# Optimization experiments

Measured on AMD Instinct MI355X. Metric: run time of the kernel, lower is better.

## Reference

```python
import jax, jax.numpy as jnp
import numpy as np

N = 50000
E = 800000
IN = 128
H = 128
OUT = 64
L = 2
THETA = 1.0
SCALE = 2.0


def setup_inputs() -> dict:
    key = jax.random.key(0)
    ks = jax.random.split(key, 12)
    g = lambda k, s: (jax.random.normal(k, s, jnp.float32) * 0.05)
    return {
        "x": jax.random.normal(ks[0], (N, IN), jnp.float32),
        "edge_index": jax.random.randint(ks[1], (2, E), 0, N),
        "mlp_w1": g(ks[2], (IN, 512)), "mlp_b1": jnp.zeros((512,), jnp.float32),
        "mlp_w2": g(ks[3], (512, 64)), "mlp_b2": jnp.zeros((64,), jnp.float32),
        "mlp_w3": g(ks[4], (64, OUT)), "mlp_b3": jnp.zeros((OUT,), jnp.float32),
        "parsing": jnp.ones((L, OUT, OUT), jnp.float32) / SCALE,
        "lin0_w": g(ks[5], (IN, H)), "lin0_b": jnp.zeros((H,), jnp.float32),
        "lin1_w": g(ks[6], (H, OUT)), "lin1_b": jnp.zeros((OUT,), jnp.float32),
        "conv_w1": g(ks[7], (L, H, H)),
        "conv_w2": g(ks[8], (L, H, H)),
    }


def reference(x, edge_index, mlp_w1, mlp_b1, mlp_w2, mlp_b2, mlp_w3, mlp_b3,
              parsing, lin0_w, lin0_b, lin1_w, lin1_b, conv_w1, conv_w2):
    row, col = edge_index[0], edge_index[1]  # start, end

    # --- learn_soft_edge3 (algebraically exact reduction of outer-product + bmm + diag) ---
    h = jax.nn.relu(x @ mlp_w1 + mlp_b1)
    h = jax.nn.relu(h @ mlp_w2 + mlp_b2)
    logits = h @ mlp_w3 + mlp_b3                      # [N, OUT]
    P = jax.nn.relu(SCALE * parsing[0])               # [OUT, OUT]
    # diag(outer(start,end) @ P)[e,c] = start[e,c] * (end @ P)[e,c]
    ew = jnp.sum(logits[row] * (logits @ P)[col], axis=1)  # [E]
    mean = ew.mean()
    var = jnp.var(ew, ddof=1)                          # torch.var is unbiased
    ew = (ew - mean) * jnp.sqrt(jnp.float32(1e-4) / var) + 1.0

    # --- GCN2 stack ---
    x0 = jax.nn.relu(x @ lin0_w + lin0_b)              # [N, H]
    # gcn_norm with self loops (weight 1)
    loop = jnp.arange(N)
    r = jnp.concatenate([row, loop])
    c = jnp.concatenate([col, loop])
    w = jnp.concatenate([ew, jnp.ones((N,), ew.dtype)])
    deg = jax.ops.segment_sum(w, c, num_segments=N)
    dinv = jnp.where(deg > 0, jax.lax.rsqrt(jnp.where(deg > 0, deg, 1.0)), 0.0)
    norm = dinv[r] * w * dinv[c]                       # [E+N]

    hcur = x0
    alpha = 0.0
    for ln in range(L):
        agg = jax.ops.segment_sum(norm[:, None] * hcur[r], c, num_segments=N)  # [N, H]
        agg = agg * (1.0 - alpha)
        x0a = alpha * x0
        beta = float(np.log(THETA / (ln + 1) + 1.0))
        out = (1.0 - beta) * agg + beta * (agg @ conv_w1[ln]) \
            + (1.0 - beta) * x0a + beta * (x0a @ conv_w2[ln])
        hcur = jax.nn.relu(out)
    return hcur @ lin1_w + lin1_b                      # [N, OUT]
```

## Files before the change

### kernel.cpp

```cpp
#include <hip/hip_runtime.h>
#include <hip/hip_bf16.h>
#include <hip/hip_fp16.h>
#include <math.h>

#define NN 50000
#define NE 800000

typedef __attribute__((ext_vector_type(8))) short bf16x8;
typedef __attribute__((ext_vector_type(4))) float f32x4;

__device__ __forceinline__ short f2bf(float f){
  unsigned u = __float_as_uint(f);
  unsigned r = (u + 0x7fffu + ((u >> 16) & 1u)) >> 16;
  return (short)r;
}
__device__ __forceinline__ float bf2f(short s){
  return __uint_as_float(((unsigned)(unsigned short)s) << 16);
}

__device__ __forceinline__ unsigned f2fp8(float f){
  __half h = __float2half(f * 0.00390625f);
  unsigned hb = (unsigned)__half_as_ushort(h);
  unsigned s = hb >> 15;
  unsigned mag = hb & 0x7fffu;
  mag = mag + 0x3fu + ((mag >> 7) & 1u);
  unsigned m8 = mag >> 7;
  if (m8 > 0x7eu) m8 = 0x7eu;
  return (s << 7) | m8;
}
__device__ __forceinline__ void fp8x4_dec(unsigned u, float2& lo, float2& hi){
  unsigned l = ((u & 0x80u) << 8) | ((u & 0x7fu) << 7)
             | ((u & 0x8000u) << 16) | ((u & 0x7f00u) << 15);
  unsigned h = ((u & 0x800000u) >> 8) | ((u & 0x7f0000u) >> 9)
             | (u & 0x80000000u) | ((u & 0x7f000000u) >> 1);
  __half2 hl = *(__half2*)&l;
  __half2 hh = *(__half2*)&h;
  lo = __half22float2(hl);
  hi = __half22float2(hh);
}
__device__ __forceinline__ float fp8_dot4(unsigned a, unsigned b){
  float2 al, ah, bl, bh;
  fp8x4_dec(a, al, ah); fp8x4_dec(b, bl, bh);
  return al.x*bl.x + al.y*bl.y + ah.x*bh.x + ah.y*bh.y;
}

__global__ __launch_bounds__(256) void zero_cnt_k(int* __restrict__ cnt, float* __restrict__ scal, int n){
  int i = blockIdx.x*256 + threadIdx.x;
  if (i < n) cnt[i] = 0;
  if (blockIdx.x == 0 && threadIdx.x < 16) scal[threadIdx.x] = 0.0f;
}

__global__ __launch_bounds__(256) void prep_k(const float* __restrict__ w1,
    const float* __restrict__ w2, const float* __restrict__ w3, const float* __restrict__ pars,
    const float* __restrict__ lin0w, const float* __restrict__ cw1, const float* __restrict__ lin1w,
    short* __restrict__ w1t, short* __restrict__ w2t, short* __restrict__ w3t, short* __restrict__ Pt,
    short* __restrict__ lin0wt, short* __restrict__ cw1t0, short* __restrict__ cw1t1,
    short* __restrict__ lin1wt){
  int idx = blockIdx.x*256 + threadIdx.x;
  if (idx < 65536){
    int n = idx >> 7, k = idx & 127;
    w1t[idx] = f2bf(w1[k*512 + n]);
  } else if (idx < 98304){
    int i = idx - 65536; int n = i >> 9, k = i & 511;
    w2t[i] = f2bf(w2[k*64 + n]);
  } else if (idx < 102400){
    int i = idx - 98304; int n = i >> 6, k = i & 63;
    w3t[i] = f2bf(w3[k*64 + n]);
  } else if (idx < 106496){
    int i = idx - 102400; int n = i >> 6, k = i & 63;
    Pt[i] = f2bf(fmaxf(2.f*pars[k*64 + n], 0.f));
  } else if (idx < 122880){
    int i = idx - 106496; int n = i >> 7, k = i & 127;
    lin0wt[i] = f2bf(lin0w[k*128 + n]);
  } else if (idx < 139264){
    int i = idx - 122880; int n = i >> 7, k = i & 127;
    cw1t0[i] = f2bf(cw1[k*128 + n]);
  } else if (idx < 155648){
    int i = idx - 139264; int n = i >> 7, k = i & 127;
    cw1t1[i] = f2bf(cw1[16384 + k*128 + n]);
  } else if (idx < 163840){
    int i = idx - 155648; int n = i >> 7, k = i & 127;
    lin1wt[i] = f2bf(lin1w[k*64 + n]);
  }
}

__global__ __launch_bounds__(256) void mlp_mfma_k(
    const float* __restrict__ x,
    const short* __restrict__ w1t, const float* __restrict__ b1,
    const short* __restrict__ w2t, const float* __restrict__ b2,
    const short* __restrict__ w3t, const float* __restrict__ b3,
    const short* __restrict__ Pt,
    unsigned char* __restrict__ lg8, unsigned char* __restrict__ lgp8,
    short* __restrict__ xb, int M)
{
  __shared__ short xs [32][136];
  __shared__ short h1s[32][520];
  __shared__ short h2s[32][72];
  __shared__ short lgs[32][72];
  const int t = threadIdx.x;
  const int wave = t >> 6, lane = t & 63;
  const int quad = lane >> 4, l16 = lane & 15;
  const int m0 = blockIdx.x * 32;

  for (int task = t; task < 512; task += 256){
    int row = task >> 4, c0 = (task & 15) * 8;
    float4 v0 = make_float4(0,0,0,0), v1 = v0;
    if (m0 + row < M){
      v0 = *(const float4*)(x + (size_t)(m0+row)*128 + c0);
      v1 = *(const float4*)(x + (size_t)(m0+row)*128 + c0 + 4);
    }
    bf16x8 s;
    s[0]=f2bf(v0.x); s[1]=f2bf(v0.y); s[2]=f2bf(v0.z); s[3]=f2bf(v0.w);
    s[4]=f2bf(v1.x); s[5]=f2bf(v1.y); s[6]=f2bf(v1.z); s[7]=f2bf(v1.w);
    *(bf16x8*)&xs[row][c0] = s;
  }
  __syncthreads();

  {
    f32x4 acc[2][8];
    #pragma unroll
    for (int mt=0;mt<2;mt++)
      #pragma unroll
      for (int nt=0;nt<8;nt++) acc[mt][nt] = (f32x4){0.f,0.f,0.f,0.f};
    for (int k0 = 0; k0 < 128; k0 += 32){
      bf16x8 a0 = *(const bf16x8*)&xs[l16     ][k0 + quad*8];
      bf16x8 a1 = *(const bf16x8*)&xs[16 + l16][k0 + quad*8];
      #pragma unroll
      for (int nt = 0; nt < 8; nt++){
        int n = wave*128 + nt*16 + l16;
        bf16x8 b = *(const bf16x8*)(w1t + (size_t)n*128 + k0 + quad*8);
        acc[0][nt] = __builtin_amdgcn_mfma_f32_16x16x32_bf16(a0, b, acc[0][nt], 0,0,0);
        acc[1][nt] = __builtin_amdgcn_mfma_f32_16x16x32_bf16(a1, b, acc[1][nt], 0,0,0);
      }
    }
    #pragma unroll
    for (int nt = 0; nt < 8; nt++){
      int n = wave*128 + nt*16 + l16;
      float bb = b1[n];
      #pragma unroll
      for (int mt = 0; mt < 2; mt++){
        #pragma unroll
        for (int r = 0; r < 4; r++){
          int row = mt*16 + quad*4 + r;
          h1s[row][n] = f2bf(fmaxf(acc[mt][nt][r] + bb, 0.f));
        }
      }
    }
  }
  __syncthreads();

  {
    f32x4 acc[2];
    acc[0] = (f32x4){0.f,0.f,0.f,0.f}; acc[1] = acc[0];
    const int n = wave*16 + l16;
    for (int k0 = 0; k0 < 512; k0 += 32){
      bf16x8 b  = *(const bf16x8*)(w2t + (size_t)n*512 + k0 + quad*8);
      bf16x8 a0 = *(const bf16x8*)&h1s[l16     ][k0 + quad*8];
      bf16x8 a1 = *(const bf16x8*)&h1s[16 + l16][k0 + quad*8];
      acc[0] = __builtin_amdgcn_mfma_f32_16x16x32_bf16(a0, b, acc[0], 0,0,0);
      acc[1] = __builtin_amdgcn_mfma_f32_16x16x32_bf16(a1, b, acc[1], 0,0,0);
    }
    float bb = b2[n];
    #pragma unroll
    for (int mt = 0; mt < 2; mt++)
      #pragma unroll
      for (int r = 0; r < 4; r++)
        h2s[mt*16 + quad*4 + r][n] = f2bf(fmaxf(acc[mt][r] + bb, 0.f));
  }
  __syncthreads();

  {
    f32x4 acc[2];
    acc[0] = (f32x4){0.f,0.f,0.f,0.f}; acc[1] = acc[0];
    const int n = wave*16 + l16;
    for (int k0 = 0; k0 < 64; k0 += 32){
      bf16x8 b  = *(const bf16x8*)(w3t + (size_t)n*64 + k0 + quad*8);
      bf16x8 a0 = *(const bf16x8*)&h2s[l16     ][k0 + quad*8];
      bf16x8 a1 = *(const bf16x8*)&h2s[16 + l16][k0 + quad*8];
      acc[0] = __builtin_amdgcn_mfma_f32_16x16x32_bf16(a0, b, acc[0], 0,0,0);
      acc[1] = __builtin_amdgcn_mfma_f32_16x16x32_bf16(a1, b, acc[1], 0,0,0);
    }
    float bb = b3[n];
    #pragma unroll
    for (int mt = 0; mt < 2; mt++)
      #pragma unroll
      for (int r = 0; r < 4; r++)
        lgs[mt*16 + quad*4 + r][n] = f2bf(acc[mt][r] + bb);
  }
  __syncthreads();

  {
    f32x4 acc[2];
    acc[0] = (f32x4){0.f,0.f,0.f,0.f}; acc[1] = acc[0];
    const int n = wave*16 + l16;
    for (int k0 = 0; k0 < 64; k0 += 32){
      bf16x8 b  = *(const bf16x8*)(Pt + (size_t)n*64 + k0 + quad*8);
      bf16x8 a0 = *(const bf16x8*)&lgs[l16     ][k0 + quad*8];
      bf16x8 a1 = *(const bf16x8*)&lgs[16 + l16][k0 + quad*8];
      acc[0] = __builtin_amdgcn_mfma_f32_16x16x32_bf16(a0, b, acc[0], 0,0,0);
      acc[1] = __builtin_amdgcn_mfma_f32_16x16x32_bf16(a1, b, acc[1], 0,0,0);
    }
    #pragma unroll
    for (int mt = 0; mt < 2; mt++)
      #pragma unroll
      for (int r = 0; r < 4; r++)
        h2s[mt*16 + quad*4 + r][n] = f2bf(acc[mt][r]);
  }
  __syncthreads();

  {
    int row = t >> 3, c0 = (t & 7) * 8;
    int gm = m0 + row;
    if (gm < M){
      const short* pl = &lgs[row][c0];
      const short* pp = &h2s[row][c0];
      unsigned a0 = 0, a1 = 0, b0 = 0, b1 = 0;
      #pragma unroll
      for (int j = 0; j < 4; j++){
        a0 |= f2fp8(bf2f(pl[j]))     << (8*j);
        a1 |= f2fp8(bf2f(pl[4+j]))   << (8*j);
        b0 |= f2fp8(bf2f(pp[j]))     << (8*j);
        b1 |= f2fp8(bf2f(pp[4+j]))   << (8*j);
      }
      uint2 av; av.x = a0; av.y = a1;
      uint2 bv; bv.x = b0; bv.y = b1;
      *(uint2*)(lg8  + (size_t)gm*64 + c0) = av;
      *(uint2*)(lgp8 + (size_t)gm*64 + c0) = bv;
    }
  }
  for (int task = t; task < 512; task += 256){
    int row = task >> 4, c0 = (task & 15) * 8;
    int gm = m0 + row;
    if (gm < M)
      *(bf16x8*)(xb + (size_t)gm*128 + c0) = *(const bf16x8*)&xs[row][c0];
  }
}

template<int NT, bool RELU, bool RESID, bool BF16OUT>
__global__ __launch_bounds__(256) void bgemm_k(
    const short* __restrict__ A, const short* __restrict__ Bt,
    const float* __restrict__ bias, const short* __restrict__ extra,
    float* __restrict__ C, short* __restrict__ Cb, int M, float beta)
{
  const int N = NT*64;
  __shared__ short As[32][136];
  const int t = threadIdx.x;
  const int wave = t >> 6, lane = t & 63;
  const int quad = lane >> 4, l16 = lane & 15;
  const int m0 = blockIdx.x * 32;

  for (int task = t; task < 512; task += 256){
    int row = task >> 4, c0 = (task & 15) * 8;
    bf16x8 v = {0,0,0,0,0,0,0,0};
    if (m0 + row < M) v = *(const bf16x8*)(A + (size_t)(m0+row)*128 + c0);
    *(bf16x8*)&As[row][c0] = v;
  }
  __syncthreads();

  f32x4 acc[2][NT];
  #pragma unroll
  for (int mt=0;mt<2;mt++)
    #pragma unroll
    for (int nt=0;nt<NT;nt++) acc[mt][nt] = (f32x4){0.f,0.f,0.f,0.f};

  #pragma unroll
  for (int k0 = 0; k0 < 128; k0 += 32){
    bf16x8 a0 = *(const bf16x8*)&As[l16     ][k0 + quad*8];
    bf16x8 a1 = *(const bf16x8*)&As[16 + l16][k0 + quad*8];
    #pragma unroll
    for (int nt = 0; nt < NT; nt++){
      int n = (wave*NT + nt)*16 + l16;
      bf16x8 b = *(const bf16x8*)(Bt + (size_t)n*128 + k0 + quad*8);
      acc[0][nt] = __builtin_amdgcn_mfma_f32_16x16x32_bf16(a0, b, acc[0][nt], 0,0,0);
      acc[1][nt] = __builtin_amdgcn_mfma_f32_16x16x32_bf16(a1, b, acc[1][nt], 0,0,0);
    }
  }

  #pragma unroll
  for (int nt = 0; nt < NT; nt++){
    int n = (wave*NT + nt)*16 + l16;
    float bb = (bias != nullptr) ? bias[n] : 0.f;
    #pragma unroll
    for (int mt = 0; mt < 2; mt++){
      #pragma unroll
      for (int r = 0; r < 4; r++){
        int gm = m0 + mt*16 + quad*4 + r;
        if (gm >= M) continue;
        float v = acc[mt][nt][r];
        if (RESID){
          float ex = bf2f(extra[(size_t)gm*N + n]);
          v = beta*v + (1.f - beta)*ex;
        }
        v += bb;
        if (RELU) v = fmaxf(v, 0.f);
        if (BF16OUT) Cb[(size_t)gm*N + n] = f2bf(v);
        else         C [(size_t)gm*N + n] = v;
      }
    }
  }
}

__global__ __launch_bounds__(256) void count_k(const int* __restrict__ col, int* __restrict__ cnt,
    int* __restrict__ rank, int E){
  int i = (blockIdx.x*256 + threadIdx.x)*4;
  if (i + 3 < E){
    int4 c = *(const int4*)(col + i);
    int r0 = atomicAdd(&cnt[c.x], 1);
    int r1 = atomicAdd(&cnt[c.y], 1);
    int r2 = atomicAdd(&cnt[c.z], 1);
    int r3 = atomicAdd(&cnt[c.w], 1);
    *(int4*)(rank + i) = make_int4(r0, r1, r2, r3);
  } else {
    for (; i < E; i++) rank[i] = atomicAdd(&cnt[col[i]], 1);
  }
}

__global__ __launch_bounds__(256) void scan_sums_k(const int* __restrict__ cnt, int* __restrict__ bsum, int n){
  __shared__ int s[256];
  const int t = threadIdx.x;
  int i = blockIdx.x*1024 + t*4;
  int4 v = make_int4(0,0,0,0);
  if (i + 3 < n) v = *(const int4*)(cnt + i);
  else {
    if (i   < n) v.x = cnt[i];
    if (i+1 < n) v.y = cnt[i+1];
    if (i+2 < n) v.z = cnt[i+2];
    if (i+3 < n) v.w = cnt[i+3];
  }
  s[t] = v.x + v.y + v.z + v.w;
  __syncthreads();
  for (int st = 128; st; st >>= 1){
    if (t < st) s[t] += s[t + st];
    __syncthreads();
  }
  if (t == 0) bsum[blockIdx.x] = s[0];
}

__global__ __launch_bounds__(64) void scan_bsum_k(int* __restrict__ bsum, int nb){
  int t = threadIdx.x;
  int own = (t < nb) ? bsum[t] : 0;
  int v = own;
  #pragma unroll
  for (int off = 1; off < 64; off <<= 1){
    int o = __shfl_up(v, off, 64);
    if (t >= off) v += o;
  }
  if (t < nb) bsum[t] = v - own;
}

__global__ __launch_bounds__(256) void scan_final_k(const int* __restrict__ cnt, const int* __restrict__ bsum,
    int* __restrict__ off, int n, int total){
  __shared__ int s[256];
  const int t = threadIdx.x;
  int i = blockIdx.x*1024 + t*4;
  int4 v = make_int4(0,0,0,0);
  if (i + 3 < n) v = *(const int4*)(cnt + i);
  else {
    if (i   < n) v.x = cnt[i];
    if (i+1 < n) v.y = cnt[i+1];
    if (i+2 < n) v.z = cnt[i+2];
    if (i+3 < n) v.w = cnt[i+3];
  }
  int tsum = v.x + v.y + v.z + v.w;
  s[t] = tsum;
  __syncthreads();
  #pragma unroll
  for (int st = 1; st < 256; st <<= 1){
    int a = (t >= st) ? s[t - st] : 0;
    __syncthreads();
    s[t] += a;
    __syncthreads();
  }
  int base = s[t] - tsum + bsum[blockIdx.x];
  int o0 = base, o1 = o0 + v.x, o2 = o1 + v.y, o3 = o2 + v.z;
  if (i   < n) off[i]   = o0;
  if (i+1 < n) off[i+1] = o1;
  if (i+2 < n) off[i+2] = o2;
  if (i+3 < n) off[i+3] = o3;
  if (blockIdx.x == 0 && t == 0) off[n] = total;
}

__global__ __launch_bounds__(256) void scatter_k(const int* __restrict__ row, const int* __restrict__ col,
    const int* __restrict__ off, const int* __restrict__ rank,
    int2* __restrict__ csr_sd, int E){
  int i = (blockIdx.x*256 + threadIdx.x)*4;
  if (i + 3 < E){
    int4 r = *(const int4*)(row + i);
    int4 c = *(const int4*)(col + i);
    int4 k = *(const int4*)(rank + i);
    int o0 = off[c.x], o1 = off[c.y], o2 = off[c.z], o3 = off[c.w];
    int2 p0; p0.x = r.x; p0.y = c.x;
    int2 p1; p1.x = r.y; p1.y = c.y;
    int2 p2; p2.x = r.z; p2.y = c.z;
    int2 p3; p3.x = r.w; p3.y = c.w;
    csr_sd[o0 + k.x] = p0;
    csr_sd[o1 + k.y] = p1;
    csr_sd[o2 + k.z] = p2;
    csr_sd[o3 + k.w] = p3;
  } else {
    for (; i < E; i++){
      int2 p; p.x = row[i]; p.y = col[i];
      csr_sd[off[col[i]] + rank[i]] = p;
    }
  }
}

__global__ __launch_bounds__(256) void ew2_k(const unsigned char* __restrict__ lg8,
    const unsigned char* __restrict__ lgp8,
    const int2* __restrict__ sd,
    float* __restrict__ w, float* __restrict__ scal, int E){
  const int t = threadIdx.x;
  const int lane = t & 63, wid = t >> 6;
  const int g = lane >> 4, q = lane & 15;
  const int gid = (blockIdx.x*4 + wid)*4 + g;
  const int ngroups = gridDim.x*16;
  float s = 0.f, ss = 0.f;
  for (int base = gid*4; base < E; base += ngroups*4){
    int4 p01 = *(const int4*)(sd + base);
    int4 p23 = *(const int4*)(sd + base + 2);
    unsigned a0 = *(const unsigned*)(lg8  + (size_t)p01.x*64 + q*4);
    unsigned a1 = *(const unsigned*)(lg8  + (size_t)p01.z*64 + q*4);
    unsigned a2 = *(const unsigned*)(lg8  + (size_t)p23.x*64 + q*4);
    unsigned a3 = *(const unsigned*)(lg8  + (size_t)p23.z*64 + q*4);
    unsigned b0 = *(const unsigned*)(lgp8 + (size_t)p01.y*64 + q*4);
    unsigned b1 = *(const unsigned*)(lgp8 + (size_t)p01.w*64 + q*4);
    unsigned b2 = *(const unsigned*)(lgp8 + (size_t)p23.y*64 + q*4);
    unsigned b3 = *(const unsigned*)(lgp8 + (size_t)p23.w*64 + q*4);
    float v0 = fp8_dot4(a0, b0);
    float v1 = fp8_dot4(a1, b1);
    float v2 = fp8_dot4(a2, b2);
    float v3 = fp8_dot4(a3, b3);
    #pragma unroll
    for (int o = 1; o < 16; o <<= 1){
      v0 += __shfl_xor(v0, o); v1 += __shfl_xor(v1, o);
      v2 += __shfl_xor(v2, o); v3 += __shfl_xor(v3, o);
    }
    if (q == 0){
      float4 vv = make_float4(v0*65536.f, v1*65536.f, v2*65536.f, v3*65536.f);
      *(float4*)(w + base) = vv;
      s  += vv.x + vv.y + vv.z + vv.w;
      ss += vv.x*vv.x + vv.y*vv.y + vv.z*vv.z + vv.w*vv.w;
    }
  }
  #pragma unroll
  for (int o = 1; o < 64; o <<= 1){ s += __shfl_xor(s, o); ss += __shfl_xor(ss, o); }
  __shared__ float ls[4], lss[4];
  if (lane == 0){ ls[wid] = s; lss[wid] = ss; }
  __syncthreads();
  if (t == 0){
    atomicAdd(&scal[0], ls[0]+ls[1]+ls[2]+ls[3]);
    atomicAdd(&scal[1], lss[0]+lss[1]+lss[2]+lss[3]);
  }
}

__global__ void finalize_k(float* scal, int E){
  double sum = (double)scal[0], sumsq = (double)scal[1];
  double mean = sum / (double)E;
  double var  = (sumsq - sum*sum/(double)E) / (double)(E-1);
  scal[2] = (float)mean;
  scal[3] = (float)sqrt(1e-4 / var);
}

__global__ __launch_bounds__(256) void degnorm_k(float* __restrict__ w, const int* __restrict__ off,
    const float* __restrict__ scal, float* __restrict__ dinv, int Nn){
  int n = blockIdx.x*256 + threadIdx.x;
  if (n < Nn){
    float mean = scal[2], k = scal[3];
    int s = off[n], e = off[n+1];
    float d = 1.0f;
    for (int j = s; j < e; j++){
      float v = (w[j] - mean) * k + 1.0f;
      w[j] = v;
      d += v;
    }
    dinv[n] = (d > 0.f) ? rsqrtf(d) : 0.f;
  }
}

__global__ __launch_bounds__(256) void wfin_k(float* __restrict__ w, const int2* __restrict__ sd,
    const float* __restrict__ dinv, int E){
  int i = (blockIdx.x*256 + threadIdx.x)*4;
  if (i + 3 < E){
    int4 p01 = *(const int4*)(sd + i);
    int4 p23 = *(const int4*)(sd + i + 2);
    float4 wv = *(const float4*)(w + i);
    float d0 = dinv[p01.x]*dinv[p01.y];
    float d1 = dinv[p01.z]*dinv[p01.w];
    float d2 = dinv[p23.x]*dinv[p23.y];
    float d3 = dinv[p23.z]*dinv[p23.w];
    wv.x *= d0; wv.y *= d1; wv.z *= d2; wv.w *= d3;
    *(float4*)(w + i) = wv;
  } else {
    for (; i < E; i++){
      int2 p = sd[i];
      w[i] = w[i] * dinv[p.y] * dinv[p.x];
    }
  }
}

__global__ __launch_bounds__(256) void agg_gather_k(const short* __restrict__ hb,
    const int* __restrict__ off, const int2* __restrict__ sd, const float* __restrict__ w,
    const float* __restrict__ dinv, short* __restrict__ aggb, int Nn){
  int n = blockIdx.x*4 + (threadIdx.x >> 6);
  int lane = threadIdx.x & 63;
  if (n >= Nn) return;
  float d = dinv[n];
  short2 hv = *(const short2*)(hb + (size_t)n*128 + lane*2);
  float acc0 = d*d*bf2f(hv.x), acc1 = d*d*bf2f(hv.y);
  int s = off[n], e = off[n+1];
  int j = s;
  for (; j + 7 < e; j += 8){
    int4 p0 = *(const int4*)(sd + j);
    int4 p1 = *(const int4*)(sd + j + 2);
    int4 p2 = *(const int4*)(sd + j + 4);
    int4 p3 = *(const int4*)(sd + j + 6);
    float4 w0 = *(const float4*)(w + j);
    float4 w1 = *(const float4*)(w + j + 4);
    short2 h0 = *(const short2*)(hb + (size_t)p0.x*128 + lane*2);
    short2 h1 = *(const short2*)(hb + (size_t)p0.z*128 + lane*2);
    short2 h2 = *(const short2*)(hb + (size_t)p1.x*128 + lane*2);
    short2 h3 = *(const short2*)(hb + (size_t)p1.z*128 + lane*2);
    short2 h4 = *(const short2*)(hb + (size_t)p2.x*128 + lane*2);
    short2 h5 = *(const short2*)(hb + (size_t)p2.z*128 + lane*2);
    short2 h6 = *(const short2*)(hb + (size_t)p3.x*128 + lane*2);
    short2 h7 = *(const short2*)(hb + (size_t)p3.z*128 + lane*2);
    acc0 += w0.x*bf2f(h0.x) + w0.y*bf2f(h1.x) + w0.z*bf2f(h2.x) + w0.w*bf2f(h3.x)
          + w1.x*bf2f(h4.x) + w1.y*bf2f(h5.x) + w1.z*bf2f(h6.x) + w1.w*bf2f(h7.x);
    acc1 += w0.x*bf2f(h0.y) + w0.y*bf2f(h1.y) + w0.z*bf2f(h2.y) + w0.w*bf2f(h3.y)
          + w1.x*bf2f(h4.y) + w1.y*bf2f(h5.y) + w1.z*bf2f(h6.y) + w1.w*bf2f(h7.y);
  }
  for (; j < e; j++){
    int2 p = sd[j];
    short2 h0 = *(const short2*)(hb + (size_t)p.x*128 + lane*2);
    float w0 = w[j];
    acc0 += w0*bf2f(h0.x); acc1 += w0*bf2f(h0.y);
  }
  short2 o; o.x = f2bf(acc0); o.y = f2bf(acc1);
  *(short2*)(aggb + (size_t)n*128 + lane*2) = o;
}

extern "C" void kernel_launch(void* const* d_in, const int* in_sizes, int n_in,
                              void* d_out, int out_size, void* d_ws, size_t ws_size,
                              hipStream_t stream){
  const float* x      = (const float*)d_in[0];
  const int*   ei     = (const int*)  d_in[1];
  const float* w1     = (const float*)d_in[2];
  const float* b1     = (const float*)d_in[3];
  const float* w2     = (const float*)d_in[4];
  const float* b2     = (const float*)d_in[5];
  const float* w3     = (const float*)d_in[6];
  const float* b3     = (const float*)d_in[7];
  const float* pars   = (const float*)d_in[8];
  const float* lin0w  = (const float*)d_in[9];
  const float* lin0b  = (const float*)d_in[10];
  const float* lin1w  = (const float*)d_in[11];
  const float* lin1b  = (const float*)d_in[12];
  const float* cw1    = (const float*)d_in[13];
  float* out          = (float*)d_out;

  float* ws = (float*)d_ws;
  int*   cnt     = (int*)(ws + 0);
  int*   off     = (int*)(ws + 50048);
  int2*  csr_sd  = (int2*)(ws + 150144);
  int*   bsum    = (int*)(ws + 1750400);
  short* lin0wt  = (short*)(ws + 1751000);
  short* cw1t0   = lin0wt + 16384;
  short* cw1t1   = cw1t0 + 16384;
  short* lin1wt  = cw1t1 + 16384;
  unsigned char* lg8  = (unsigned char*)(ws + 1800000);
  unsigned char* lgp8 = (unsigned char*)(ws + 2600000);
  float* csr_w2  = ws + 3400000;
  float* dinv    = ws + 5800000;
  float* scal    = ws + 5850048;
  short* bufAb   = (short*)(ws + 5900000);
  short* bufCb   = (short*)(ws + 9100000);
  short* aggb    = (short*)(ws + 12300000);
  short* bufBb   = (short*)(ws + 15500000);
  short* w1t     = (short*)(ws + 18700000);
  short* w2t     = w1t + 65536;
  short* w3t     = w2t + 32768;
  short* Pt      = w3t + 4096;
  short* xb      = (short*)(ws + 18800000);
  int*   rank    = (int*)(ws + 22000000);

  const int Mn = NN, E = NE;
  const int* erow = ei;
  const int* ecol = ei + E;
  const float beta0 = 0.69314718055994530942f;
  const float beta1 = 0.40546510810816438198f;
  const int nScanB = (Mn + 1023) / 1024;
  const int nGB = (Mn + 31) / 32;
  const int nE4 = (E/4 + 255) / 256;

  zero_cnt_k<<<(Mn+255)/256, 256, 0, stream>>>(cnt, scal, Mn);
  prep_k<<<(163840+255)/256, 256, 0, stream>>>(w1, w2, w3, pars, lin0w, cw1, lin1w,
                                               w1t, w2t, w3t, Pt, lin0wt, cw1t0, cw1t1, lin1wt);
  count_k<<<nE4, 256, 0, stream>>>(ecol, cnt, rank, E);
  scan_sums_k<<<nScanB, 256, 0, stream>>>(cnt, bsum, Mn);
  scan_bsum_k<<<1, 64, 0, stream>>>(bsum, nScanB);
  scan_final_k<<<nScanB, 256, 0, stream>>>(cnt, bsum, off, Mn, E);
  scatter_k<<<nE4, 256, 0, stream>>>(erow, ecol, off, rank, csr_sd, E);
  mlp_mfma_k<<<(Mn+31)/32, 256, 0, stream>>>(x, w1t, b1, w2t, b2, w3t, b3, Pt,
                                             lg8, lgp8, xb, Mn);
  ew2_k<<<1024, 256, 0, stream>>>(lg8, lgp8, csr_sd, csr_w2, scal, E);
  finalize_k<<<1, 1, 0, stream>>>(scal, E);
  degnorm_k<<<(Mn+255)/256, 256, 0, stream>>>(csr_w2, off, scal, dinv, Mn);
  wfin_k<<<nE4, 256, 0, stream>>>(csr_w2, csr_sd, dinv, E);
  bgemm_k<2,true,false,true><<<nGB, 256, 0, stream>>>(xb, lin0wt, lin0b, nullptr, nullptr, bufAb, Mn, 0.f);
  agg_gather_k<<<(Mn+3)/4, 256, 0, stream>>>(bufAb, off, csr_sd, csr_w2, dinv, aggb, Mn);
  bgemm_k<2,true,true,true><<<nGB, 256, 0, stream>>>(aggb, cw1t0, nullptr, aggb, nullptr, bufCb, Mn, beta0);
  agg_gather_k<<<(Mn+3)/4, 256, 0, stream>>>(bufCb, off, csr_sd, csr_w2, dinv, aggb, Mn);
  bgemm_k<2,true,true,true><<<nGB, 256, 0, stream>>>(aggb, cw1t1, nullptr, aggb, nullptr, bufBb, Mn, beta1);
  bgemm_k<1,false,false,false><<<nGB, 256, 0, stream>>>(bufBb, lin1wt, lin1b, nullptr, out, nullptr, Mn, 0.f);
}
```

Measured before the change: 397.6 us.

## Split MLP hidden layer into two halves to shrink LDS and accumulators

The fused MLP kernel now computes the 512-wide first hidden layer in two 256-column halves. Each half is consumed immediately into the second-layer accumulators, so the hidden-activation shared buffer halves and per-wave accumulator registers drop from 16 to 8 vectors. This aims to raise occupancy in the first stage of the pipeline. The bf16 copy of x is now written straight from registers during the load instead of a separate pass at the end. The cost is extra barriers and two passes over the second-layer loop.

```diff
diff --git a/kernel.cpp b/kernel.cpp
--- a/kernel.cpp
+++ b/kernel.cpp
@@ -94,7 +94,7 @@
     short* __restrict__ xb, int M)
 {
   __shared__ short xs [32][136];
-  __shared__ short h1s[32][520];
+  __shared__ short h1s[32][264];
   __shared__ short h2s[32][72];
   __shared__ short lgs[32][72];
   const int t = threadIdx.x;
@@ -105,96 +105,104 @@
   for (int task = t; task < 512; task += 256){
     int row = task >> 4, c0 = (task & 15) * 8;
     float4 v0 = make_float4(0,0,0,0), v1 = v0;
-    if (m0 + row < M){
-      v0 = *(const float4*)(x + (size_t)(m0+row)*128 + c0);
-      v1 = *(const float4*)(x + (size_t)(m0+row)*128 + c0 + 4);
+    int gm = m0 + row;
+    if (gm < M){
+      v0 = *(const float4*)(x + (size_t)gm*128 + c0);
+      v1 = *(const float4*)(x + (size_t)gm*128 + c0 + 4);
     }
     bf16x8 s;
     s[0]=f2bf(v0.x); s[1]=f2bf(v0.y); s[2]=f2bf(v0.z); s[3]=f2bf(v0.w);
     s[4]=f2bf(v1.x); s[5]=f2bf(v1.y); s[6]=f2bf(v1.z); s[7]=f2bf(v1.w);
     *(bf16x8*)&xs[row][c0] = s;
-  }
-  __syncthreads();
-
-  {
-    f32x4 acc[2][8];
-    #pragma unroll
-    for (int mt=0;mt<2;mt++)
-      #pragma unroll
-      for (int nt=0;nt<8;nt++) acc[mt][nt] = (f32x4){0.f,0.f,0.f,0.f};
-    for (int k0 = 0; k0 < 128; k0 += 32){
-      bf16x8 a0 = *(const bf16x8*)&xs[l16     ][k0 + quad*8];
-      bf16x8 a1 = *(const bf16x8*)&xs[16 + l16][k0 + quad*8];
-      #pragma unroll
-      for (int nt = 0; nt < 8; nt++){
-        int n = wave*128 + nt*16 + l16;
-        bf16x8 b = *(const bf16x8*)(w1t + (size_t)n*128 + k0 + quad*8);
-        acc[0][nt] = __builtin_amdgcn_mfma_f32_16x16x32_bf16(a0, b, acc[0][nt], 0,0,0);
-        acc[1][nt] = __builtin_amdgcn_mfma_f32_16x16x32_bf16(a1, b, acc[1][nt], 0,0,0);
-      }
-    }
-    #pragma unroll
-    for (int nt = 0; nt < 8; nt++){
-      int n = wave*128 + nt*16 + l16;
-      float bb = b1[n];
-      #pragma unroll
-      for (int mt = 0; mt < 2; mt++){
+    if (gm < M) *(bf16x8*)(xb + (size_t)gm*128 + c0) = s;
+  }
+  __syncthreads();
+
+  f32x4 acc2[2];
+  acc2[0] = (f32x4){0.f,0.f,0.f,0.f}; acc2[1] = acc2[0];
+  const int n2 = wave*16 + l16;
+
+  #pragma unroll
+  for (int half = 0; half < 2; half++){
+    {
+      f32x4 acc[2][4];
+      #pragma unroll
+      for (int mt=0;mt<2;mt++)
         #pragma unroll
-        for (int r = 0; r < 4; r++){
-          int row = mt*16 + quad*4 + r;
-          h1s[row][n] = f2bf(fmaxf(acc[mt][nt][r] + bb, 0.f));
+        for (int nt=0;nt<4;nt++) acc[mt][nt] = (f32x4){0.f,0.f,0.f,0.f};
+      #pragma unroll
+      for (int k0 = 0; k0 < 128; k0 += 32){
+        bf16x8 a0 = *(const bf16x8*)&xs[l16     ][k0 + quad*8];
+        bf16x8 a1 = *(const bf16x8*)&xs[16 + l16][k0 + quad*8];
+        #pragma unroll
+        for (int nt = 0; nt < 4; nt++){
+          int n = half*256 + wave*64 + nt*16 + l16;
+          bf16x8 b = *(const bf16x8*)(w1t + (size_t)n*128 + k0 + quad*8);
+          acc[0][nt] = __builtin_amdgcn_mfma_f32_16x16x32_bf16(a0, b, acc[0][nt], 0,0,0);
+          acc[1][nt] = __builtin_amdgcn_mfma_f32_16x16x32_bf16(a1, b, acc[1][nt], 0,0,0);
         }
       }
-    }
+      #pragma unroll
+      for (int nt = 0; nt < 4; nt++){
+        int n  = half*256 + wave*64 + nt*16 + l16;
+        int cl = wave*64 + nt*16 + l16;
+        float bb = b1[n];
+        #pragma unroll
+        for (int mt = 0; mt < 2; mt++){
+          #pragma unroll
+          for (int r = 0; r < 4; r++){
+            int row = mt*16 + quad*4 + r;
+            h1s[row][cl] = f2bf(fmaxf(acc[mt][nt][r] + bb, 0.f));
+          }
+        }
+      }
+    }
+    __syncthreads();
+
+    for (int k0 = 0; k0 < 256; k0 += 32){
+      bf16x8 b  = *(const bf16x8*)(w2t + (size_t)n2*512 + half*256 + k0 + quad*8);
+      bf16x8 a0 = *(const bf16x8*)&h1s[l16     ][k0 + quad*8];
+      bf16x8 a1 = *(const bf16x8*)&h1s[16 + l16][k0 + quad*8];
+      acc2[0] = __builtin_amdgcn_mfma_f32_16x16x32_bf16(a0, b, acc2[0], 0,0,0);
+      acc2[1] = __builtin_amdgcn_mfma_f32_16x16x32_bf16(a1, b, acc2[1], 0,0,0);
+    }
+    if (half == 0) __syncthreads();
+  }
+
+  {
+    float bb = b2[n2];
+    #pragma unroll
+    for (int mt = 0; mt < 2; mt++)
+      #pragma unroll
+      for (int r = 0; r < 4; r++)
+        h2s[mt*16 + quad*4 + r][n2] = f2bf(fmaxf(acc2[mt][r] + bb, 0.f));
   }
   __syncthreads();
 
   {
     f32x4 acc[2];
     acc[0] = (f32x4){0.f,0.f,0.f,0.f}; acc[1] = acc[0];
-    const int n = wave*16 + l16;
-    for (int k0 = 0; k0 < 512; k0 += 32){
-      bf16x8 b  = *(const bf16x8*)(w2t + (size_t)n*512 + k0 + quad*8);
-      bf16x8 a0 = *(const bf16x8*)&h1s[l16     ][k0 + quad*8];
-      bf16x8 a1 = *(const bf16x8*)&h1s[16 + l16][k0 + quad*8];
-      acc[0] = __builtin_amdgcn_mfma_f32_16x16x32_bf16(a0, b, acc[0], 0,0,0);
-      acc[1] = __builtin_amdgcn_mfma_f32_16x16x32_bf16(a1, b, acc[1], 0,0,0);
-    }
-    float bb = b2[n];
-    #pragma unroll
-    for (int mt = 0; mt < 2; mt++)
-      #pragma unroll
-      for (int r = 0; r < 4; r++)
-        h2s[mt*16 + quad*4 + r][n] = f2bf(fmaxf(acc[mt][r] + bb, 0.f));
-  }
-  __syncthreads();
-
-  {
-    f32x4 acc[2];
-    acc[0] = (f32x4){0.f,0.f,0.f,0.f}; acc[1] = acc[0];
-    const int n = wave*16 + l16;
     for (int k0 = 0; k0 < 64; k0 += 32){
-      bf16x8 b  = *(const bf16x8*)(w3t + (size_t)n*64 + k0 + quad*8);
+      bf16x8 b  = *(const bf16x8*)(w3t + (size_t)n2*64 + k0 + quad*8);
       bf16x8 a0 = *(const bf16x8*)&h2s[l16     ][k0 + quad*8];
       bf16x8 a1 = *(const bf16x8*)&h2s[16 + l16][k0 + quad*8];
       acc[0] = __builtin_amdgcn_mfma_f32_16x16x32_bf16(a0, b, acc[0], 0,0,0);
       acc[1] = __builtin_amdgcn_mfma_f32_16x16x32_bf16(a1, b, acc[1], 0,0,0);
     }
-    float bb = b3[n];
+    float bb = b3[n2];
     #pragma unroll
     for (int mt = 0; mt < 2; mt++)
       #pragma unroll
       for (int r = 0; r < 4; r++)
-        lgs[mt*16 + quad*4 + r][n] = f2bf(acc[mt][r] + bb);
+        lgs[mt*16 + quad*4 + r][n2] = f2bf(acc[mt][r] + bb);
   }
   __syncthreads();
 
   {
     f32x4 acc[2];
     acc[0] = (f32x4){0.f,0.f,0.f,0.f}; acc[1] = acc[0];
-    const int n = wave*16 + l16;
     for (int k0 = 0; k0 < 64; k0 += 32){
-      bf16x8 b  = *(const bf16x8*)(Pt + (size_t)n*64 + k0 + quad*8);
+      bf16x8 b  = *(const bf16x8*)(Pt + (size_t)n2*64 + k0 + quad*8);
       bf16x8 a0 = *(const bf16x8*)&lgs[l16     ][k0 + quad*8];
       bf16x8 a1 = *(const bf16x8*)&lgs[16 + l16][k0 + quad*8];
       acc[0] = __builtin_amdgcn_mfma_f32_16x16x32_bf16(a0, b, acc[0], 0,0,0);
@@ -204,7 +212,7 @@
     for (int mt = 0; mt < 2; mt++)
       #pragma unroll
       for (int r = 0; r < 4; r++)
-        h2s[mt*16 + quad*4 + r][n] = f2bf(acc[mt][r]);
+        h2s[mt*16 + quad*4 + r][n2] = f2bf(acc[mt][r]);
   }
   __syncthreads();
 
@@ -227,12 +235,6 @@
       *(uint2*)(lg8  + (size_t)gm*64 + c0) = av;
       *(uint2*)(lgp8 + (size_t)gm*64 + c0) = bv;
     }
-  }
-  for (int task = t; task < 512; task += 256){
-    int row = task >> 4, c0 = (task & 15) * 8;
-    int gm = m0 + row;
-    if (gm < M)
-      *(bf16x8*)(xb + (size_t)gm*128 + c0) = *(const bf16x8*)&xs[row][c0];
   }
 }
 
```

After: 395.9 us. Within noise of the previous version (-0.4%).
